# Optimization experiments

Measured on AMD Instinct MI355X. Metric: run time of the kernel, lower is better.

## Reference

```python
import jax, jax.numpy as jnp
import numpy as np

N, LP, LD, D, H, GS = 16, 2048, 512, 256, 8, 4
HD = D // H           # head_size = 32
TAU = 1.0             # softmax_tau
ITERS = 4             # sinkhorn_iters
INF = 1.0e6


def setup_inputs() -> dict:
    key = jax.random.key(0)
    ks = jax.random.split(key, 10)
    inp = {
        "protein": jax.random.normal(ks[0], (N, LP, D), jnp.float32),
        "drug": jax.random.normal(ks[1], (N, LD, D), jnp.float32),
        "mask_prot": jax.random.bernoulli(ks[2], 0.9, (N, LP)),
        "mask_drug": jax.random.bernoulli(ks[3], 0.9, (N, LD)),
    }
    names = ["Wq_p", "Wk_p", "Wv_p", "Wq_d", "Wk_d", "Wv_d"]
    for i, name in enumerate(names):
        inp[name] = jax.random.normal(ks[4 + i], (D, D), jnp.float32) * (1.0 / np.sqrt(D))
    return inp


def _group(x, mask):
    n, L, d = x.shape
    g = L // GS
    xg = x.reshape(n, g, GS, d).mean(2)          # [N,G,D]
    mg = mask.reshape(n, g, GS).any(2)           # [N,G]
    return xg, mg


def _alpha_logits(logits, mask_row, mask_col):
    # logits: [N,L1,L2,H]; sinkhorn normalization as in the torch module
    n, L1, L2, h = logits.shape
    logits = logits * (1.0 / np.sqrt(HD))
    pair = mask_row[:, :, None, None] & mask_col[:, None, :, None]  # [N,L1,L2,1]
    logits = jnp.where(pair, logits, logits - INF)
    A = jax.nn.softmax((logits / TAU).reshape(n, L1 * L2, h), axis=1).reshape(n, L1, L2, h)
    valid = pair.astype(A.dtype)
    A = A * valid + 1e-12 * valid
    for _ in range(ITERS):
        row_sum = (A * valid).sum(2, keepdims=True) + 1e-12
        A = A / row_sum * valid
        col_sum = (A * valid).sum(1, keepdims=True) + 1e-12
        A = A / col_sum * valid
    return A * valid


def _proj(x, W):
    n, g, d = x.shape
    return (x @ W.T).reshape(n, g, H, HD)


def reference(protein, drug, mask_prot, mask_drug, Wq_p, Wk_p, Wv_p, Wq_d, Wk_d, Wv_d):
    pg, mp = _group(protein, mask_prot)   # [N,Gp,D], [N,Gp]
    dg, md = _group(drug, mask_drug)      # [N,Gd,D], [N,Gd]

    qp, kp, vp = _proj(pg, Wq_p), _proj(pg, Wk_p), _proj(pg, Wv_p)
    qd, kd, vd = _proj(dg, Wq_d), _proj(dg, Wk_d), _proj(dg, Wv_d)

    att = lambda q, k: jnp.einsum('blhd,bkhd->blkh', q, k)
    a_pp = _alpha_logits(att(qp, kp), mp, mp)
    a_pd = _alpha_logits(att(qp, kd), mp, md)
    a_dp = _alpha_logits(att(qd, kp), md, mp)
    a_dd = _alpha_logits(att(qd, kd), md, md)

    mix = lambda a, v: jnp.einsum('blkh,bkhd->blhd', a, v).reshape(a.shape[0], a.shape[1], D)
    prot_embedding = (mix(a_pp, vp) + mix(a_pd, vd)) * 0.5  # [N,Gp,D]
    drug_embedding = (mix(a_dp, vp) + mix(a_dd, vd)) * 0.5  # [N,Gd,D]

    # agg_mode == 'mean': masked mean over valid groups
    mpf = mp[..., None].astype(prot_embedding.dtype)
    mdf = md[..., None].astype(drug_embedding.dtype)
    prot_embed = (prot_embedding * mpf).sum(1) / mpf.sum(1)
    drug_embed = (drug_embedding * mdf).sum(1) / mdf.sum(1)

    query_embed = jnp.concatenate([prot_embed, drug_embed], axis=1)  # [N,2D]
    return query_embed, a_dp
```

## Files before the change

kernel.cpp:

```cpp
#include <hip/hip_runtime.h>
#include <hip/hip_bf16.h>

#define NB   16
#define DT   256
#define HT   8
#define HDT  32
#define GP   512
#define GD   128

using bf16x8 = __attribute__((ext_vector_type(8))) short;
using f32x4  = __attribute__((ext_vector_type(4))) float;

__device__ __forceinline__ short f2bf(float f) {
  __hip_bfloat16 h = __float2bfloat16(f);
  short s; __builtin_memcpy(&s, &h, 2);
  return s;
}

extern "C" __global__ __launch_bounds__(256)
void k_group(const float* __restrict__ protein, const float* __restrict__ drug,
             const int* __restrict__ mprot, const int* __restrict__ mdrug,
             const float* __restrict__ Wk, const float* __restrict__ Wq,
             short* __restrict__ pg_bf, short* __restrict__ dg_bf,
             int* __restrict__ mp_g, int* __restrict__ md_g,
             short* __restrict__ Wk_bf, short* __restrict__ Wq_bf,
             float* __restrict__ part, int* __restrict__ cntp) {
  int b = blockIdx.x;
  int t = threadIdx.x;
  if (b >= 320) {
    int base = (b - 320) * 512;
    #pragma unroll
    for (int j = 0; j < 2; ++j) {
      int gid = base + t + j * 256;
      if (gid < 65536) Wk_bf[gid] = f2bf(Wk[gid]);
      else             Wq_bf[gid - 65536] = f2bf(Wq[gid - 65536]);
    }
    return;
  }
  int n, c0, G;
  const float* src; const int* msk; short* dst; int* mg;
  if (b < 256) { n = b >> 4; c0 = (b & 15) * 32; G = GP;
                 src = protein; msk = mprot; dst = pg_bf; mg = mp_g; }
  else { int bb = b - 256; n = bb >> 2; c0 = (bb & 3) * 32; G = GD;
         src = drug; msk = mdrug; dst = dg_bf; mg = md_g; }

  __shared__ int gmask[32];
  if (t < 32) {
    const int* m = msk + ((size_t)n * G + c0 + t) * 4;
    int v = (m[0] | m[1] | m[2] | m[3]) ? 1 : 0;
    gmask[t] = v;
    mg[n * G + c0 + t] = v;
  }
  __syncthreads();
  if (t == 0) {
    int c = 0;
    #pragma unroll
    for (int i = 0; i < 32; ++i) c += gmask[i];
    cntp[b] = c;
  }

  float acc_s = 0.f;
  const float* bp = src + ((size_t)n * G + c0) * 1024 + t;
  #pragma unroll 4
  for (int gi = 0; gi < 32; ++gi) {
    const float* rp = bp + (size_t)gi * 1024;
    float gm = 0.25f * (rp[0] + rp[256] + rp[512] + rp[768]);
    dst[((size_t)n * G + c0 + gi) * 256 + t] = f2bf(gm);
    if (gmask[gi]) acc_s += gm;
  }
  part[(size_t)b * 256 + t] = acc_s;
}

extern "C" __global__ __launch_bounds__(256)
void k_proj_embed(const short* __restrict__ pg_bf, const short* __restrict__ dg_bf,
                  const short* __restrict__ Wk_bf, const short* __restrict__ Wq_bf,
                  short* __restrict__ kp_bf, short* __restrict__ qd_bf,
                  const float* __restrict__ part, const int* __restrict__ cntp,
                  const float* __restrict__ Wvp, const float* __restrict__ Wvd,
                  float* __restrict__ out) {
  int b = blockIdx.x;
  int t = threadIdx.x;
  if (b >= 160) {
    int bb = b - 160;
    int n = bb >> 3;
    int dchunk = (bb & 7) * 32;
    __shared__ float sps[256], sds[256];
    float a1 = 0.f;
    #pragma unroll
    for (int i = 0; i < 16; ++i) a1 += part[(size_t)(n * 16 + i) * 256 + t];
    sps[t] = a1;
    float a2 = 0.f;
    #pragma unroll
    for (int i = 0; i < 4; ++i) a2 += part[(size_t)(256 + n * 4 + i) * 256 + t];
    sds[t] = a2;
    __syncthreads();
    int cp = 0, cd = 0;
    #pragma unroll
    for (int i = 0; i < 16; ++i) cp += cntp[n * 16 + i];
    #pragma unroll
    for (int i = 0; i < 4; ++i) cd += cntp[256 + n * 4 + i];
    int dloc = t >> 3, ks = (t & 7) * 32;
    int d = dchunk + dloc;
    const float* wp = Wvp + (size_t)d * 256 + ks;
    const float* wd = Wvd + (size_t)d * 256 + ks;
    float acc = 0.f;
    #pragma unroll
    for (int k = 0; k < 32; k += 4) {
      float4 a = *(const float4*)(wp + k);
      float4 c = *(const float4*)(wd + k);
      acc += sps[ks + k] * a.x + sps[ks + k + 1] * a.y + sps[ks + k + 2] * a.z + sps[ks + k + 3] * a.w
           + sds[ks + k] * c.x + sds[ks + k + 1] * c.y + sds[ks + k + 2] * c.z + sds[ks + k + 3] * c.w;
    }
    #pragma unroll
    for (int m = 1; m <= 4; m <<= 1) acc += __shfl_xor(acc, m, 64);
    if ((t & 7) == 0) {
      acc *= 0.5f;
      out[n * 512 + d]       = acc / (float)cp;
      out[n * 512 + 256 + d] = acc / (float)cd;
    }
    return;
  }
  int w = t >> 6, lane = t & 63;
  int c15 = lane & 15, g = lane >> 4;
  const short *A, *W; short* o; int rt;
  if (b < 128) { A = pg_bf; W = Wk_bf; o = kp_bf; rt = b * 4 + w; }
  else         { A = dg_bf; W = Wq_bf; o = qd_bf; rt = (b - 128) * 4 + w; }

  const short* ap = A + ((size_t)rt * 16 + c15) * 256;
  f32x4 acc[16];
  #pragma unroll
  for (int i = 0; i < 16; ++i) acc[i] = (f32x4){0.f, 0.f, 0.f, 0.f};

  #pragma unroll
  for (int ks = 0; ks < 8; ++ks) {
    bf16x8 af = *(const bf16x8*)(ap + ks * 32 + g * 8);
    #pragma unroll
    for (int ct = 0; ct < 16; ++ct) {
      bf16x8 bfr = *(const bf16x8*)(W + ((size_t)(ct * 16 + c15)) * 256 + ks * 32 + g * 8);
      acc[ct] = __builtin_amdgcn_mfma_f32_16x16x32_bf16(af, bfr, acc[ct], 0, 0, 0);
    }
  }
  #pragma unroll
  for (int ct = 0; ct < 16; ++ct) {
    #pragma unroll
    for (int r = 0; r < 4; ++r) {
      o[((size_t)rt * 16 + 4 * g + r) * 256 + ct * 16 + c15] = f2bf(acc[ct][r]);
    }
  }
}

extern "C" __global__ __launch_bounds__(512)
void k_scalars(const short* __restrict__ qd, const short* __restrict__ kp,
               const int* __restrict__ md_g, const int* __restrict__ mp_g,
               float* __restrict__ rcz) {
  int bid = blockIdx.x;
  int n = ((bid & 7) << 1) | ((bid >> 3) & 1);
  int h = bid >> 4;
  int tid = threadIdx.x;
  int w = tid >> 6, lane = tid & 63;
  int c15 = lane & 15, g = lane >> 4;

  __shared__ float c_s[GP];
  __shared__ float r_s[GD];
  __shared__ float t_s[GD];
  __shared__ float red[8][GP];
  __shared__ float z_sh, sr_sh, sc_sh, kv_sh;
  __shared__ int mp_sh[GP];
  __shared__ int md_sh[GD];

  if (tid < GP) { int m = mp_g[n * GP + tid]; mp_sh[tid] = m; c_s[tid] = m ? 1.f : 0.f; }
  if (tid < GD) { int m = md_g[n * GD + tid]; md_sh[tid] = m; r_s[tid] = m ? 1.f : 0.f; }
  __syncthreads();

  if (w == 0) {
    float v = (float)(mp_sh[lane] + mp_sh[lane + 64] + mp_sh[lane + 128] + mp_sh[lane + 192] +
                      mp_sh[lane + 256] + mp_sh[lane + 320] + mp_sh[lane + 384] + mp_sh[lane + 448]);
    #pragma unroll
    for (int m = 1; m <= 32; m <<= 1) v += __shfl_xor(v, m, 64);
    if (lane == 0) kv_sh = v;
  }

  int qrow = 16 * w + c15;
  bf16x8 af = *(const bf16x8*)(qd + ((size_t)(n * GD + qrow)) * 256 + h * HDT + g * 8);

  _Float16 p[32][4];
  #pragma unroll
  for (int ct = 0; ct < 32; ++ct) {
    int krow = 16 * ct + c15;
    bf16x8 bfr = *(const bf16x8*)(kp + ((size_t)(n * GP + krow)) * 256 + h * HDT + g * 8);
    f32x4 acc = __builtin_amdgcn_mfma_f32_16x16x32_bf16(af, bfr, (f32x4){0.f,0.f,0.f,0.f}, 0, 0, 0);
    int mcol = mp_sh[16 * ct + c15];
    #pragma unroll
    for (int r = 0; r < 4; ++r) {
      int row = 16 * w + 4 * g + r;
      p[ct][r] = (_Float16)((mcol && md_sh[row]) ? __expf(acc[r] * 0.17677669529663687f) : 0.f);
    }
  }

  {
    float pa0 = 0.f, pa1 = 0.f, pa2 = 0.f, pa3 = 0.f;
    #pragma unroll
    for (int ct = 0; ct < 32; ++ct) {
      pa0 += (float)p[ct][0]; pa1 += (float)p[ct][1];
      pa2 += (float)p[ct][2]; pa3 += (float)p[ct][3];
    }
    #pragma unroll
    for (int m = 1; m <= 8; m <<= 1) {
      pa0 += __shfl_xor(pa0, m, 64); pa1 += __shfl_xor(pa1, m, 64);
      pa2 += __shfl_xor(pa2, m, 64); pa3 += __shfl_xor(pa3, m, 64);
    }
    if (c15 == 0) t_s[16 * w + 4 * g + 0] = pa0;
    if (c15 == 1) t_s[16 * w + 4 * g + 1] = pa1;
    if (c15 == 2) t_s[16 * w + 4 * g + 2] = pa2;
    if (c15 == 3) t_s[16 * w + 4 * g + 3] = pa3;
  }
  __syncthreads();
  if (w == 0) {
    float v = t_s[lane] + t_s[lane + 64];
    #pragma unroll
    for (int m = 1; m <= 32; m <<= 1) v += __shfl_xor(v, m, 64);
    if (lane == 0) z_sh = v;
  }
  __syncthreads();
  float Zinv = 1.0f / z_sh;
  float Sc = kv_sh;

  #pragma unroll 1
  for (int it = 0; it < 4; ++it) {
    if (tid < GD) {
      float ti = t_s[tid] * Zinv + 1e-12f * Sc;
      float ri = r_s[tid];
      r_s[tid] = md_sh[tid] ? (ri / (ri * ti + 1e-12f)) : 0.f;
    }
    __syncthreads();
    if (w == 0) {
      float v = r_s[lane] + r_s[lane + 64];
      #pragma unroll
      for (int m = 1; m <= 32; m <<= 1) v += __shfl_xor(v, m, 64);
      if (lane == 0) sr_sh = v;
    }
    __syncthreads();
    float Sr = sr_sh;
    float rr0 = r_s[16 * w + 4 * g + 0];
    float rr1 = r_s[16 * w + 4 * g + 1];
    float rr2 = r_s[16 * w + 4 * g + 2];
    float rr3 = r_s[16 * w + 4 * g + 3];
    #pragma unroll
    for (int ct = 0; ct < 32; ++ct) {
      float u = (float)p[ct][0] * rr0 + (float)p[ct][1] * rr1 +
                (float)p[ct][2] * rr2 + (float)p[ct][3] * rr3;
      u += __shfl_xor(u, 16, 64);
      u += __shfl_xor(u, 32, 64);
      if (g == 0) red[w][16 * ct + c15] = u;
    }
    __syncthreads();
    {
      float cs = red[0][tid] + red[1][tid] + red[2][tid] + red[3][tid] +
                 red[4][tid] + red[5][tid] + red[6][tid] + red[7][tid];
      float uj = cs * Zinv + 1e-12f * Sr;
      float cj = c_s[tid];
      c_s[tid] = mp_sh[tid] ? (cj / (cj * uj + 1e-12f)) : 0.f;
    }
    __syncthreads();
    if (w == 0) {
      float v = c_s[lane] + c_s[lane + 64] + c_s[lane + 128] + c_s[lane + 192] +
                c_s[lane + 256] + c_s[lane + 320] + c_s[lane + 384] + c_s[lane + 448];
      #pragma unroll
      for (int m = 1; m <= 32; m <<= 1) v += __shfl_xor(v, m, 64);
      if (lane == 0) sc_sh = v;
    }
    __syncthreads();
    Sc = sc_sh;
    if (it < 3) {
      float pa0 = 0.f, pa1 = 0.f, pa2 = 0.f, pa3 = 0.f;
      #pragma unroll
      for (int ct = 0; ct < 32; ++ct) {
        float cv = c_s[16 * ct + c15];
        pa0 += (float)p[ct][0] * cv; pa1 += (float)p[ct][1] * cv;
        pa2 += (float)p[ct][2] * cv; pa3 += (float)p[ct][3] * cv;
      }
      #pragma unroll
      for (int m = 1; m <= 8; m <<= 1) {
        pa0 += __shfl_xor(pa0, m, 64); pa1 += __shfl_xor(pa1, m, 64);
        pa2 += __shfl_xor(pa2, m, 64); pa3 += __shfl_xor(pa3, m, 64);
      }
      if (c15 == 0) t_s[16 * w + 4 * g + 0] = pa0;
      if (c15 == 1) t_s[16 * w + 4 * g + 1] = pa1;
      if (c15 == 2) t_s[16 * w + 4 * g + 2] = pa2;
      if (c15 == 3) t_s[16 * w + 4 * g + 3] = pa3;
      __syncthreads();
    }
  }

  size_t rb = (size_t)(n * 8 + h) * 1024;
  if (tid < GD) rcz[rb + tid] = r_s[tid];
  if (tid < GP) rcz[rb + 128 + tid] = c_s[tid];
  if (tid == 0) rcz[rb + 640] = Zinv;
}

extern "C" __global__ __launch_bounds__(256)
void k_write(const short* __restrict__ qd, const short* __restrict__ kp,
             const float* __restrict__ rcz, float* __restrict__ out) {
  int bid = blockIdx.x;
  int n = ((bid & 7) << 1) | ((bid >> 3) & 1);
  int rest = bid >> 4;
  int rt = rest >> 2;
  int cc = rest & 3;
  int w = threadIdx.x >> 6, lane = threadIdx.x & 63;
  int c15 = lane & 15, g = lane >> 4;

  const short* qbase = qd + ((size_t)(n * GD + rt * 16 + c15)) * 256;
  bf16x8 af[8];
  #pragma unroll
  for (int h = 0; h < 8; ++h) af[h] = *(const bf16x8*)(qbase + h * HDT + g * 8);

  size_t rb = (size_t)n * 8 * 1024;
  float rv[8][4], zin[8];
  #pragma unroll
  for (int h = 0; h < 8; ++h) {
    const float* rp = rcz + rb + (size_t)h * 1024;
    #pragma unroll
    for (int r = 0; r < 4; ++r) rv[h][r] = rp[rt * 16 + 4 * g + r];
    zin[h] = rp[640];
  }

  #pragma unroll
  for (int ct = 0; ct < 2; ++ct) {
    int col = cc * 128 + w * 32 + ct * 16 + c15;
    f32x4 acc[8]; float cw[8];
    #pragma unroll
    for (int h = 0; h < 8; ++h) {
      bf16x8 bfr = *(const bf16x8*)(kp + ((size_t)(n * GP + col)) * 256 + h * HDT + g * 8);
      acc[h] = __builtin_amdgcn_mfma_f32_16x16x32_bf16(af[h], bfr, (f32x4){0.f,0.f,0.f,0.f}, 0, 0, 0);
      cw[h] = rcz[rb + (size_t)h * 1024 + 128 + col];
    }
    #pragma unroll
    for (int r = 0; r < 4; ++r) {
      int row = rt * 16 + 4 * g + r;
      float4 lo, hi;
      lo.x = rv[0][r] * (__expf(acc[0][r] * 0.17677669529663687f) * zin[0] + 1e-12f) * cw[0];
      lo.y = rv[1][r] * (__expf(acc[1][r] * 0.17677669529663687f) * zin[1] + 1e-12f) * cw[1];
      lo.z = rv[2][r] * (__expf(acc[2][r] * 0.17677669529663687f) * zin[2] + 1e-12f) * cw[2];
      lo.w = rv[3][r] * (__expf(acc[3][r] * 0.17677669529663687f) * zin[3] + 1e-12f) * cw[3];
      hi.x = rv[4][r] * (__expf(acc[4][r] * 0.17677669529663687f) * zin[4] + 1e-12f) * cw[4];
      hi.y = rv[5][r] * (__expf(acc[5][r] * 0.17677669529663687f) * zin[5] + 1e-12f) * cw[5];
      hi.z = rv[6][r] * (__expf(acc[6][r] * 0.17677669529663687f) * zin[6] + 1e-12f) * cw[6];
      hi.w = rv[7][r] * (__expf(acc[7][r] * 0.17677669529663687f) * zin[7] + 1e-12f) * cw[7];
      float* dst = out + 8192 + (((size_t)(n * GD + row)) * GP + col) * 8;
      *(float4*)dst = lo;
      *(float4*)(dst + 4) = hi;
    }
  }
}

extern "C" void kernel_launch(void* const* d_in, const int* in_sizes, int n_in,
                              void* d_out, int out_size, void* d_ws, size_t ws_size,
                              hipStream_t stream) {
  const float* protein = (const float*)d_in[0];
  const float* drug    = (const float*)d_in[1];
  const int*   mprot   = (const int*)d_in[2];
  const int*   mdrug   = (const int*)d_in[3];
  const float* Wk_p = (const float*)d_in[5];
  const float* Wv_p = (const float*)d_in[6];
  const float* Wq_d = (const float*)d_in[7];
  const float* Wv_d = (const float*)d_in[9];
  float* out = (float*)d_out;

  char* wsb = (char*)d_ws;
  short* pg_bf = (short*)wsb;                 wsb += (size_t)NB * GP * 256 * 2;
  short* dg_bf = (short*)wsb;                 wsb += (size_t)NB * GD * 256 * 2;
  short* kp_bf = (short*)wsb;                 wsb += (size_t)NB * GP * 256 * 2;
  short* qd_bf = (short*)wsb;                 wsb += (size_t)NB * GD * 256 * 2;
  short* Wk_bf = (short*)wsb;                 wsb += 65536 * 2;
  short* Wq_bf = (short*)wsb;                 wsb += 65536 * 2;
  float* part  = (float*)wsb;                 wsb += (size_t)320 * 256 * 4;
  float* rcz   = (float*)wsb;                 wsb += (size_t)128 * 1024 * 4;
  int*   cntp  = (int*)wsb;                   wsb += 320 * 4;
  int*   mp_g  = (int*)wsb;                   wsb += 8192 * 4;
  int*   md_g  = (int*)wsb;                   wsb += 2048 * 4;

  k_group<<<576, 256, 0, stream>>>(protein, drug, mprot, mdrug, Wk_p, Wq_d,
                                   pg_bf, dg_bf, mp_g, md_g, Wk_bf, Wq_bf,
                                   part, cntp);
  k_proj_embed<<<288, 256, 0, stream>>>(pg_bf, dg_bf, Wk_bf, Wq_bf, kp_bf, qd_bf,
                                        part, cntp, Wv_p, Wv_d, out);
  k_scalars<<<128, 512, 0, stream>>>(qd_bf, kp_bf, md_g, mp_g, rcz);
  k_write<<<512, 256, 0, stream>>>(qd_bf, kp_bf, rcz, out);
}
```

Measured before the change: 186.8 us.

## Fuse grouping into projection GEMM, widen sinkhorn kernel, merge embed into write

The grouping/mean step and the weight bf16 conversion are folded into the K/Q projection kernel, which now reads fp32 protein/drug and weights directly and accumulates masked partial sums in shared memory via atomics. The embed GEMV moves into the final write kernel as extra blocks, cutting the launch count from four to three and removing the intermediate bf16 buffers. The sinkhorn scalar kernel doubles to 1024 threads, splitting columns across two waves so each keeps 16 fp32 tiles in registers instead of 32 fp16 ones. In exchange, the projection kernel redundantly converts weights per block and runs with only 160 blocks, and the 1024-thread kernel may face register pressure.

```diff
diff --git a/kernel.cpp b/kernel.cpp
--- a/kernel.cpp
+++ b/kernel.cpp
@@ -7,6 +7,7 @@
 #define HDT  32
 #define GP   512
 #define GD   128
+#define SCL  0.17677669529663687f
 
 using bf16x8 = __attribute__((ext_vector_type(8))) short;
 using f32x4  = __attribute__((ext_vector_type(4))) float;
@@ -17,126 +18,94 @@
   return s;
 }
 
+__device__ __forceinline__ bf16x8 cvt8(float4 a, float4 b) {
+  bf16x8 r;
+  r[0] = f2bf(a.x); r[1] = f2bf(a.y); r[2] = f2bf(a.z); r[3] = f2bf(a.w);
+  r[4] = f2bf(b.x); r[5] = f2bf(b.y); r[6] = f2bf(b.z); r[7] = f2bf(b.w);
+  return r;
+}
+
 extern "C" __global__ __launch_bounds__(256)
-void k_group(const float* __restrict__ protein, const float* __restrict__ drug,
-             const int* __restrict__ mprot, const int* __restrict__ mdrug,
-             const float* __restrict__ Wk, const float* __restrict__ Wq,
-             short* __restrict__ pg_bf, short* __restrict__ dg_bf,
-             int* __restrict__ mp_g, int* __restrict__ md_g,
-             short* __restrict__ Wk_bf, short* __restrict__ Wq_bf,
-             float* __restrict__ part, int* __restrict__ cntp) {
-  int b = blockIdx.x;
-  int t = threadIdx.x;
-  if (b >= 320) {
-    int base = (b - 320) * 512;
-    #pragma unroll
-    for (int j = 0; j < 2; ++j) {
-      int gid = base + t + j * 256;
-      if (gid < 65536) Wk_bf[gid] = f2bf(Wk[gid]);
-      else             Wq_bf[gid - 65536] = f2bf(Wq[gid - 65536]);
-    }
-    return;
-  }
-  int n, c0, G;
-  const float* src; const int* msk; short* dst; int* mg;
-  if (b < 256) { n = b >> 4; c0 = (b & 15) * 32; G = GP;
-                 src = protein; msk = mprot; dst = pg_bf; mg = mp_g; }
-  else { int bb = b - 256; n = bb >> 2; c0 = (bb & 3) * 32; G = GD;
-         src = drug; msk = mdrug; dst = dg_bf; mg = md_g; }
-
-  __shared__ int gmask[32];
-  if (t < 32) {
-    const int* m = msk + ((size_t)n * G + c0 + t) * 4;
+void k_fused_proj(const float* __restrict__ protein, const float* __restrict__ drug,
+                  const int* __restrict__ mprot, const int* __restrict__ mdrug,
+                  const float* __restrict__ Wk, const float* __restrict__ Wq,
+                  short* __restrict__ kp_bf, short* __restrict__ qd_bf,
+                  int* __restrict__ mp_g, int* __restrict__ md_g,
+                  float* __restrict__ part, int* __restrict__ cntp) {
+  int b = blockIdx.x, t = threadIdx.x;
+  int w = t >> 6, lane = t & 63, c15 = lane & 15, g = lane >> 4;
+  const float *src, *W; const int* msk; short* o; int* mg;
+  int bb;
+  if (b < 128) { bb = b;      src = protein; msk = mprot; W = Wk; o = kp_bf; mg = mp_g; }
+  else         { bb = b - 128; src = drug;   msk = mdrug; W = Wq; o = qd_bf; mg = md_g; }
+  int flatrow0 = bb * 64;
+
+  __shared__ int gm_s[64];
+  __shared__ float part_s[256];
+  part_s[t] = 0.f;
+  if (t < 64) {
+    const int* m = msk + (size_t)(flatrow0 + t) * 4;
     int v = (m[0] | m[1] | m[2] | m[3]) ? 1 : 0;
-    gmask[t] = v;
-    mg[n * G + c0 + t] = v;
+    gm_s[t] = v;
+    mg[flatrow0 + t] = v;
   }
   __syncthreads();
   if (t == 0) {
     int c = 0;
     #pragma unroll
-    for (int i = 0; i < 32; ++i) c += gmask[i];
+    for (int i = 0; i < 64; ++i) c += gm_s[i];
     cntp[b] = c;
   }
 
-  float acc_s = 0.f;
-  const float* bp = src + ((size_t)n * G + c0) * 1024 + t;
-  #pragma unroll 4
-  for (int gi = 0; gi < 32; ++gi) {
-    const float* rp = bp + (size_t)gi * 1024;
-    float gm = 0.25f * (rp[0] + rp[256] + rp[512] + rp[768]);
-    dst[((size_t)n * G + c0 + gi) * 256 + t] = f2bf(gm);
-    if (gmask[gi]) acc_s += gm;
-  }
-  part[(size_t)b * 256 + t] = acc_s;
-}
-
-extern "C" __global__ __launch_bounds__(256)
-void k_proj_embed(const short* __restrict__ pg_bf, const short* __restrict__ dg_bf,
-                  const short* __restrict__ Wk_bf, const short* __restrict__ Wq_bf,
-                  short* __restrict__ kp_bf, short* __restrict__ qd_bf,
-                  const float* __restrict__ part, const int* __restrict__ cntp,
-                  const float* __restrict__ Wvp, const float* __restrict__ Wvd,
-                  float* __restrict__ out) {
-  int b = blockIdx.x;
-  int t = threadIdx.x;
-  if (b >= 160) {
-    int bb = b - 160;
-    int n = bb >> 3;
-    int dchunk = (bb & 7) * 32;
-    __shared__ float sps[256], sds[256];
-    float a1 = 0.f;
-    #pragma unroll
-    for (int i = 0; i < 16; ++i) a1 += part[(size_t)(n * 16 + i) * 256 + t];
-    sps[t] = a1;
-    float a2 = 0.f;
-    #pragma unroll
-    for (int i = 0; i < 4; ++i) a2 += part[(size_t)(256 + n * 4 + i) * 256 + t];
-    sds[t] = a2;
-    __syncthreads();
-    int cp = 0, cd = 0;
-    #pragma unroll
-    for (int i = 0; i < 16; ++i) cp += cntp[n * 16 + i];
-    #pragma unroll
-    for (int i = 0; i < 4; ++i) cd += cntp[256 + n * 4 + i];
-    int dloc = t >> 3, ks = (t & 7) * 32;
-    int d = dchunk + dloc;
-    const float* wp = Wvp + (size_t)d * 256 + ks;
-    const float* wd = Wvd + (size_t)d * 256 + ks;
-    float acc = 0.f;
-    #pragma unroll
-    for (int k = 0; k < 32; k += 4) {
-      float4 a = *(const float4*)(wp + k);
-      float4 c = *(const float4*)(wd + k);
-      acc += sps[ks + k] * a.x + sps[ks + k + 1] * a.y + sps[ks + k + 2] * a.z + sps[ks + k + 3] * a.w
-           + sds[ks + k] * c.x + sds[ks + k + 1] * c.y + sds[ks + k + 2] * c.z + sds[ks + k + 3] * c.w;
-    }
-    #pragma unroll
-    for (int m = 1; m <= 4; m <<= 1) acc += __shfl_xor(acc, m, 64);
-    if ((t & 7) == 0) {
-      acc *= 0.5f;
-      out[n * 512 + d]       = acc / (float)cp;
-      out[n * 512 + 256 + d] = acc / (float)cd;
-    }
-    return;
-  }
-  int w = t >> 6, lane = t & 63;
-  int c15 = lane & 15, g = lane >> 4;
-  const short *A, *W; short* o; int rt;
-  if (b < 128) { A = pg_bf; W = Wk_bf; o = kp_bf; rt = b * 4 + w; }
-  else         { A = dg_bf; W = Wq_bf; o = qd_bf; rt = (b - 128) * 4 + w; }
-
-  const short* ap = A + ((size_t)rt * 16 + c15) * 256;
+  int grow = flatrow0 + w * 16 + c15;
+  const float* ap = src + (size_t)grow * 1024;
+  int msel = gm_s[w * 16 + c15];
+
   f32x4 acc[16];
   #pragma unroll
   for (int i = 0; i < 16; ++i) acc[i] = (f32x4){0.f, 0.f, 0.f, 0.f};
 
   #pragma unroll
   for (int ks = 0; ks < 8; ++ks) {
-    bf16x8 af = *(const bf16x8*)(ap + ks * 32 + g * 8);
+    int k0 = ks * 32 + g * 8;
+    float4 s0  = *(const float4*)(ap + k0);
+    float4 s0b = *(const float4*)(ap + k0 + 4);
+    float4 s1  = *(const float4*)(ap + 256 + k0);
+    float4 s1b = *(const float4*)(ap + 256 + k0 + 4);
+    float4 s2  = *(const float4*)(ap + 512 + k0);
+    float4 s2b = *(const float4*)(ap + 512 + k0 + 4);
+    float4 s3  = *(const float4*)(ap + 768 + k0);
+    float4 s3b = *(const float4*)(ap + 768 + k0 + 4);
+    float4 av, bv;
+    av.x = 0.25f * (s0.x + s1.x + s2.x + s3.x);
+    av.y = 0.25f * (s0.y + s1.y + s2.y + s3.y);
+    av.z = 0.25f * (s0.z + s1.z + s2.z + s3.z);
+    av.w = 0.25f * (s0.w + s1.w + s2.w + s3.w);
+    bv.x = 0.25f * (s0b.x + s1b.x + s2b.x + s3b.x);
+    bv.y = 0.25f * (s0b.y + s1b.y + s2b.y + s3b.y);
+    bv.z = 0.25f * (s0b.z + s1b.z + s2b.z + s3b.z);
+    bv.w = 0.25f * (s0b.w + s1b.w + s2b.w + s3b.w);
+    bf16x8 af = cvt8(av, bv);
+
+    float vs[8];
+    vs[0] = msel ? av.x : 0.f; vs[1] = msel ? av.y : 0.f;
+    vs[2] = msel ? av.z : 0.f; vs[3] = msel ? av.w : 0.f;
+    vs[4] = msel ? bv.x : 0.f; vs[5] = msel ? bv.y : 0.f;
+    vs[6] = msel ? bv.z : 0.f; vs[7] = msel ? bv.w : 0.f;
+    #pragma unroll
+    for (int j = 0; j < 8; ++j) {
+      #pragma unroll
+      for (int m = 1; m <= 8; m <<= 1) vs[j] += __shfl_xor(vs[j], m, 64);
+    }
+    if (c15 == 0) {
+      #pragma unroll
+      for (int j = 0; j < 8; ++j) atomicAdd(&part_s[k0 + j], vs[j]);
+    }
+
     #pragma unroll
     for (int ct = 0; ct < 16; ++ct) {
-      bf16x8 bfr = *(const bf16x8*)(W + ((size_t)(ct * 16 + c15)) * 256 + ks * 32 + g * 8);
+      const float* wp = W + (size_t)(ct * 16 + c15) * 256 + k0;
+      bf16x8 bfr = cvt8(*(const float4*)wp, *(const float4*)(wp + 4));
       acc[ct] = __builtin_amdgcn_mfma_f32_16x16x32_bf16(af, bfr, acc[ct], 0, 0, 0);
     }
   }
@@ -144,12 +113,16 @@
   for (int ct = 0; ct < 16; ++ct) {
     #pragma unroll
     for (int r = 0; r < 4; ++r) {
-      o[((size_t)rt * 16 + 4 * g + r) * 256 + ct * 16 + c15] = f2bf(acc[ct][r]);
-    }
-  }
-}
-
-extern "C" __global__ __launch_bounds__(512)
+      o[(size_t)(flatrow0 + w * 16 + 4 * g + r) * 256 + ct * 16 + c15] = f2bf(acc[ct][r]);
+    }
+  }
+  __syncthreads();
+  part[(size_t)b * 256 + t] = part_s[t];
+}
+
+#define FOR16(X) X(0) X(1) X(2) X(3) X(4) X(5) X(6) X(7) X(8) X(9) X(10) X(11) X(12) X(13) X(14) X(15)
+
+extern "C" __global__ __launch_bounds__(1024)
 void k_scalars(const short* __restrict__ qd, const short* __restrict__ kp,
                const int* __restrict__ md_g, const int* __restrict__ mp_g,
                float* __restrict__ rcz) {
@@ -157,12 +130,14 @@
   int n = ((bid & 7) << 1) | ((bid >> 3) & 1);
   int h = bid >> 4;
   int tid = threadIdx.x;
-  int w = tid >> 6, lane = tid & 63;
+  int wid = tid >> 6, lane = tid & 63;
+  int wr = wid >> 1, ch = wid & 1;
   int c15 = lane & 15, g = lane >> 4;
 
   __shared__ float c_s[GP];
   __shared__ float r_s[GD];
   __shared__ float t_s[GD];
+  __shared__ float t2[2][GD];
   __shared__ float red[8][GP];
   __shared__ float z_sh, sr_sh, sc_sh, kv_sh;
   __shared__ int mp_sh[GP];
@@ -172,7 +147,7 @@
   if (tid < GD) { int m = md_g[n * GD + tid]; md_sh[tid] = m; r_s[tid] = m ? 1.f : 0.f; }
   __syncthreads();
 
-  if (w == 0) {
+  if (wid == 0) {
     float v = (float)(mp_sh[lane] + mp_sh[lane + 64] + mp_sh[lane + 128] + mp_sh[lane + 192] +
                       mp_sh[lane + 256] + mp_sh[lane + 320] + mp_sh[lane + 384] + mp_sh[lane + 448]);
     #pragma unroll
@@ -180,42 +155,43 @@
     if (lane == 0) kv_sh = v;
   }
 
-  int qrow = 16 * w + c15;
+  int qrow = 16 * wr + c15;
   bf16x8 af = *(const bf16x8*)(qd + ((size_t)(n * GD + qrow)) * 256 + h * HDT + g * 8);
-
-  _Float16 p[32][4];
-  #pragma unroll
-  for (int ct = 0; ct < 32; ++ct) {
-    int krow = 16 * ct + c15;
-    bf16x8 bfr = *(const bf16x8*)(kp + ((size_t)(n * GP + krow)) * 256 + h * HDT + g * 8);
-    f32x4 acc = __builtin_amdgcn_mfma_f32_16x16x32_bf16(af, bfr, (f32x4){0.f,0.f,0.f,0.f}, 0, 0, 0);
-    int mcol = mp_sh[16 * ct + c15];
-    #pragma unroll
-    for (int r = 0; r < 4; ++r) {
-      int row = 16 * w + 4 * g + r;
-      p[ct][r] = (_Float16)((mcol && md_sh[row]) ? __expf(acc[r] * 0.17677669529663687f) : 0.f);
-    }
-  }
+  int row0 = 16 * wr + 4 * g;
+  int mr0 = md_sh[row0], mr1 = md_sh[row0 + 1], mr2 = md_sh[row0 + 2], mr3 = md_sh[row0 + 3];
+  const short* kbase = kp + ((size_t)n * GP) * 256 + h * HDT + g * 8;
+  int colbase = ch * 256 + c15;
+
+#define DECLP(i) f32x4 P##i;
+  FOR16(DECLP)
+#define MKP(i) { int col = colbase + 16 * (i); \
+    bf16x8 bfr = *(const bf16x8*)(kbase + (size_t)col * 256); \
+    f32x4 a = __builtin_amdgcn_mfma_f32_16x16x32_bf16(af, bfr, (f32x4){0.f,0.f,0.f,0.f}, 0, 0, 0); \
+    int mc = mp_sh[col]; \
+    P##i[0] = (mc && mr0) ? __expf(a[0] * SCL) : 0.f; \
+    P##i[1] = (mc && mr1) ? __expf(a[1] * SCL) : 0.f; \
+    P##i[2] = (mc && mr2) ? __expf(a[2] * SCL) : 0.f; \
+    P##i[3] = (mc && mr3) ? __expf(a[3] * SCL) : 0.f; }
+  FOR16(MKP)
 
   {
     float pa0 = 0.f, pa1 = 0.f, pa2 = 0.f, pa3 = 0.f;
-    #pragma unroll
-    for (int ct = 0; ct < 32; ++ct) {
-      pa0 += (float)p[ct][0]; pa1 += (float)p[ct][1];
-      pa2 += (float)p[ct][2]; pa3 += (float)p[ct][3];
-    }
+#define RS0(i) pa0 += P##i[0]; pa1 += P##i[1]; pa2 += P##i[2]; pa3 += P##i[3];
+    FOR16(RS0)
     #pragma unroll
     for (int m = 1; m <= 8; m <<= 1) {
       pa0 += __shfl_xor(pa0, m, 64); pa1 += __shfl_xor(pa1, m, 64);
       pa2 += __shfl_xor(pa2, m, 64); pa3 += __shfl_xor(pa3, m, 64);
     }
-    if (c15 == 0) t_s[16 * w + 4 * g + 0] = pa0;
-    if (c15 == 1) t_s[16 * w + 4 * g + 1] = pa1;
-    if (c15 == 2) t_s[16 * w + 4 * g + 2] = pa2;
-    if (c15 == 3) t_s[16 * w + 4 * g + 3] = pa3;
-  }
-  __syncthreads();
-  if (w == 0) {
+    if (c15 == 0) t2[ch][row0 + 0] = pa0;
+    if (c15 == 1) t2[ch][row0 + 1] = pa1;
+    if (c15 == 2) t2[ch][row0 + 2] = pa2;
+    if (c15 == 3) t2[ch][row0 + 3] = pa3;
+  }
+  __syncthreads();
+  if (tid < GD) t_s[tid] = t2[0][tid] + t2[1][tid];
+  __syncthreads();
+  if (wid == 0) {
     float v = t_s[lane] + t_s[lane + 64];
     #pragma unroll
     for (int m = 1; m <= 32; m <<= 1) v += __shfl_xor(v, m, 64);
@@ -233,7 +209,7 @@
       r_s[tid] = md_sh[tid] ? (ri / (ri * ti + 1e-12f)) : 0.f;
     }
     __syncthreads();
-    if (w == 0) {
+    if (wid == 0) {
       float v = r_s[lane] + r_s[lane + 64];
       #pragma unroll
       for (int m = 1; m <= 32; m <<= 1) v += __shfl_xor(v, m, 64);
@@ -241,20 +217,15 @@
     }
     __syncthreads();
     float Sr = sr_sh;
-    float rr0 = r_s[16 * w + 4 * g + 0];
-    float rr1 = r_s[16 * w + 4 * g + 1];
-    float rr2 = r_s[16 * w + 4 * g + 2];
-    float rr3 = r_s[16 * w + 4 * g + 3];
-    #pragma unroll
-    for (int ct = 0; ct < 32; ++ct) {
-      float u = (float)p[ct][0] * rr0 + (float)p[ct][1] * rr1 +
-                (float)p[ct][2] * rr2 + (float)p[ct][3] * rr3;
-      u += __shfl_xor(u, 16, 64);
-      u += __shfl_xor(u, 32, 64);
-      if (g == 0) red[w][16 * ct + c15] = u;
-    }
-    __syncthreads();
     {
+      float rr0 = r_s[row0], rr1 = r_s[row0 + 1], rr2 = r_s[row0 + 2], rr3 = r_s[row0 + 3];
+#define CP(i) { float u = P##i[0] * rr0 + P##i[1] * rr1 + P##i[2] * rr2 + P##i[3] * rr3; \
+      u += __shfl_xor(u, 16, 64); u += __shfl_xor(u, 32, 64); \
+      if (g == 0) red[wr][colbase + 16 * (i)] = u; }
+      FOR16(CP)
+    }
+    __syncthreads();
+    if (tid < GP) {
       float cs = red[0][tid] + red[1][tid] + red[2][tid] + red[3][tid] +
                  red[4][tid] + red[5][tid] + red[6][tid] + red[7][tid];
       float uj = cs * Zinv + 1e-12f * Sr;
@@ -262,7 +233,7 @@
       c_s[tid] = mp_sh[tid] ? (cj / (cj * uj + 1e-12f)) : 0.f;
     }
     __syncthreads();
-    if (w == 0) {
+    if (wid == 0) {
       float v = c_s[lane] + c_s[lane + 64] + c_s[lane + 128] + c_s[lane + 192] +
                 c_s[lane + 256] + c_s[lane + 320] + c_s[lane + 384] + c_s[lane + 448];
       #pragma unroll
@@ -272,23 +243,21 @@
     __syncthreads();
     Sc = sc_sh;
     if (it < 3) {
-      float pa0 = 0.f, pa1 = 0.f, pa2 = 0.f, pa3 = 0.f;
-      #pragma unroll
-      for (int ct = 0; ct < 32; ++ct) {
-        float cv = c_s[16 * ct + c15];
-        pa0 += (float)p[ct][0] * cv; pa1 += (float)p[ct][1] * cv;
-        pa2 += (float)p[ct][2] * cv; pa3 += (float)p[ct][3] * cv;
+      float qa0 = 0.f, qa1 = 0.f, qa2 = 0.f, qa3 = 0.f;
+#define RP(i) { float cv = c_s[colbase + 16 * (i)]; \
+      qa0 += P##i[0] * cv; qa1 += P##i[1] * cv; qa2 += P##i[2] * cv; qa3 += P##i[3] * cv; }
+      FOR16(RP)
+      #pragma unroll
+      for (int m = 1; m <= 8; m <<= 1) {
+        qa0 += __shfl_xor(qa0, m, 64); qa1 += __shfl_xor(qa1, m, 64);
+        qa2 += __shfl_xor(qa2, m, 64); qa3 += __shfl_xor(qa3, m, 64);
       }
-      #pragma unroll
-      for (int m = 1; m <= 8; m <<= 1) {
-        pa0 += __shfl_xor(pa0, m, 64); pa1 += __shfl_xor(pa1, m, 64);
-        pa2 += __shfl_xor(pa2, m, 64); pa3 += __shfl_xor(pa3, m, 64);
-      }
-      if (c15 == 0) t_s[16 * w + 4 * g + 0] = pa0;
-      if (c15 == 1) t_s[16 * w + 4 * g + 1] = pa1;
-      if (c15 == 2) t_s[16 * w + 4 * g + 2] = pa2;
-      if (c15 == 3) t_s[16 * w + 4 * g + 3] = pa3;
+      if (c15 == 0) t2[ch][row0 + 0] = qa0;
+      if (c15 == 1) t2[ch][row0 + 1] = qa1;
+      if (c15 == 2) t2[ch][row0 + 2] = qa2;
+      if (c15 == 3) t2[ch][row0 + 3] = qa3;
       __syncthreads();
+      if (tid < GD) t_s[tid] = t2[0][tid] + t2[1][tid];
     }
   }
 
@@ -299,14 +268,58 @@
 }
 
 extern "C" __global__ __launch_bounds__(256)
-void k_write(const short* __restrict__ qd, const short* __restrict__ kp,
-             const float* __restrict__ rcz, float* __restrict__ out) {
+void k_write_embed(const short* __restrict__ qd, const short* __restrict__ kp,
+                   const float* __restrict__ rcz,
+                   const float* __restrict__ part, const int* __restrict__ cntp,
+                   const float* __restrict__ Wvp, const float* __restrict__ Wvd,
+                   float* __restrict__ out) {
   int bid = blockIdx.x;
+  int t = threadIdx.x;
+  if (bid >= 512) {
+    int bb = bid - 512;
+    int n = bb >> 3;
+    int dchunk = (bb & 7) * 32;
+    __shared__ float sps[256], sds[256];
+    float a1 = 0.f;
+    #pragma unroll
+    for (int i = 0; i < 8; ++i) a1 += part[(size_t)(n * 8 + i) * 256 + t];
+    sps[t] = a1;
+    float a2 = 0.f;
+    #pragma unroll
+    for (int i = 0; i < 2; ++i) a2 += part[(size_t)(128 + n * 2 + i) * 256 + t];
+    sds[t] = a2;
+    __syncthreads();
+    int cp = 0, cd = 0;
+    #pragma unroll
+    for (int i = 0; i < 8; ++i) cp += cntp[n * 8 + i];
+    #pragma unroll
+    for (int i = 0; i < 2; ++i) cd += cntp[128 + n * 2 + i];
+    int dloc = t >> 3, ks = (t & 7) * 32;
+    int d = dchunk + dloc;
+    const float* wp = Wvp + (size_t)d * 256 + ks;
+    const float* wd = Wvd + (size_t)d * 256 + ks;
+    float acc = 0.f;
+    #pragma unroll
+    for (int k = 0; k < 32; k += 4) {
+      float4 a = *(const float4*)(wp + k);
+      float4 c = *(const float4*)(wd + k);
+      acc += sps[ks + k] * a.x + sps[ks + k + 1] * a.y + sps[ks + k + 2] * a.z + sps[ks + k + 3] * a.w
+           + sds[ks + k] * c.x + sds[ks + k + 1] * c.y + sds[ks + k + 2] * c.z + sds[ks + k + 3] * c.w;
+    }
+    #pragma unroll
+    for (int m = 1; m <= 4; m <<= 1) acc += __shfl_xor(acc, m, 64);
+    if ((t & 7) == 0) {
+      acc *= 0.5f;
+      out[n * 512 + d]       = acc / (float)cp;
+      out[n * 512 + 256 + d] = acc / (float)cd;
+    }
+    return;
+  }
   int n = ((bid & 7) << 1) | ((bid >> 3) & 1);
   int rest = bid >> 4;
   int rt = rest >> 2;
   int cc = rest & 3;
-  int w = threadIdx.x >> 6, lane = threadIdx.x & 63;
+  int w = t >> 6, lane = t & 63;
   int c15 = lane & 15, g = lane >> 4;
 
   const short* qbase = qd + ((size_t)(n * GD + rt * 16 + c15)) * 256;
@@ -338,14 +351,14 @@
     for (int r = 0; r < 4; ++r) {
       int row = rt * 16 + 4 * g + r;
       float4 lo, hi;
-      lo.x = rv[0][r] * (__expf(acc[0][r] * 0.17677669529663687f) * zin[0] + 1e-12f) * cw[0];
-      lo.y = rv[1][r] * (__expf(acc[1][r] * 0.17677669529663687f) * zin[1] + 1e-12f) * cw[1];
-      lo.z = rv[2][r] * (__expf(acc[2][r] * 0.17677669529663687f) * zin[2] + 1e-12f) * cw[2];
-      lo.w = rv[3][r] * (__expf(acc[3][r] * 0.17677669529663687f) * zin[3] + 1e-12f) * cw[3];
-      hi.x = rv[4][r] * (__expf(acc[4][r] * 0.17677669529663687f) * zin[4] + 1e-12f) * cw[4];
-      hi.y = rv[5][r] * (__expf(acc[5][r] * 0.17677669529663687f) * zin[5] + 1e-12f) * cw[5];
-      hi.z = rv[6][r] * (__expf(acc[6][r] * 0.17677669529663687f) * zin[6] + 1e-12f) * cw[6];
-      hi.w = rv[7][r] * (__expf(acc[7][r] * 0.17677669529663687f) * zin[7] + 1e-12f) * cw[7];
+      lo.x = rv[0][r] * (__expf(acc[0][r] * SCL) * zin[0] + 1e-12f) * cw[0];
+      lo.y = rv[1][r] * (__expf(acc[1][r] * SCL) * zin[1] + 1e-12f) * cw[1];
+      lo.z = rv[2][r] * (__expf(acc[2][r] * SCL) * zin[2] + 1e-12f) * cw[2];
+      lo.w = rv[3][r] * (__expf(acc[3][r] * SCL) * zin[3] + 1e-12f) * cw[3];
+      hi.x = rv[4][r] * (__expf(acc[4][r] * SCL) * zin[4] + 1e-12f) * cw[4];
+      hi.y = rv[5][r] * (__expf(acc[5][r] * SCL) * zin[5] + 1e-12f) * cw[5];
+      hi.z = rv[6][r] * (__expf(acc[6][r] * SCL) * zin[6] + 1e-12f) * cw[6];
+      hi.w = rv[7][r] * (__expf(acc[7][r] * SCL) * zin[7] + 1e-12f) * cw[7];
       float* dst = out + 8192 + (((size_t)(n * GD + row)) * GP + col) * 8;
       *(float4*)dst = lo;
       *(float4*)(dst + 4) = hi;
@@ -367,23 +380,17 @@
   float* out = (float*)d_out;
 
   char* wsb = (char*)d_ws;
-  short* pg_bf = (short*)wsb;                 wsb += (size_t)NB * GP * 256 * 2;
-  short* dg_bf = (short*)wsb;                 wsb += (size_t)NB * GD * 256 * 2;
   short* kp_bf = (short*)wsb;                 wsb += (size_t)NB * GP * 256 * 2;
   short* qd_bf = (short*)wsb;                 wsb += (size_t)NB * GD * 256 * 2;
-  short* Wk_bf = (short*)wsb;                 wsb += 65536 * 2;
-  short* Wq_bf = (short*)wsb;                 wsb += 65536 * 2;
-  float* part  = (float*)wsb;                 wsb += (size_t)320 * 256 * 4;
+  float* part  = (float*)wsb;                 wsb += (size_t)160 * 256 * 4;
   float* rcz   = (float*)wsb;                 wsb += (size_t)128 * 1024 * 4;
-  int*   cntp  = (int*)wsb;                   wsb += 320 * 4;
+  int*   cntp  = (int*)wsb;                   wsb += 160 * 4;
   int*   mp_g  = (int*)wsb;                   wsb += 8192 * 4;
   int*   md_g  = (int*)wsb;                   wsb += 2048 * 4;
 
-  k_group<<<576, 256, 0, stream>>>(protein, drug, mprot, mdrug, Wk_p, Wq_d,
-                                   pg_bf, dg_bf, mp_g, md_g, Wk_bf, Wq_bf,
-                                   part, cntp);
-  k_proj_embed<<<288, 256, 0, stream>>>(pg_bf, dg_bf, Wk_bf, Wq_bf, kp_bf, qd_bf,
-                                        part, cntp, Wv_p, Wv_d, out);
-  k_scalars<<<128, 512, 0, stream>>>(qd_bf, kp_bf, md_g, mp_g, rcz);
-  k_write<<<512, 256, 0, stream>>>(qd_bf, kp_bf, rcz, out);
-}
+  k_fused_proj<<<160, 256, 0, stream>>>(protein, drug, mprot, mdrug, Wk_p, Wq_d,
+                                        kp_bf, qd_bf, mp_g, md_g, part, cntp);
+  k_scalars<<<128, 1024, 0, stream>>>(qd_bf, kp_bf, md_g, mp_g, rcz);
+  k_write_embed<<<640, 256, 0, stream>>>(qd_bf, kp_bf, rcz, part, cntp,
+                                         Wv_p, Wv_d, out);
+}
```

New measurement: 186.5 us. No clear change (-0.1%).
